# Kernel tuning notes

Hardware: AMD Instinct MI355X
Metric: run time of the kernel (lower is better)

Reference implementation:

```python
import jax, jax.numpy as jnp
import numpy as np

N_NODES = 100000
EPS = 1e-12  # F.normalize default eps


def _sage_conv(x, edge_index, Wl, bl, Wr):
    # PyG SAGEConv, aggr='mean', normalize=True.
    # edge_index[0] = source j, edge_index[1] = target i; messages flow j -> i.
    src, dst = edge_index[0], edge_index[1]
    msg_sum = jax.ops.segment_sum(x[src], dst, num_segments=N_NODES)  # [N, F]
    cnt = jax.ops.segment_sum(jnp.ones_like(src, dtype=x.dtype), dst,
                              num_segments=N_NODES)                  # [N]
    mean = msg_sum / jnp.maximum(cnt, 1.0)[:, None]  # empty neighborhoods -> 0
    out = mean @ Wl + bl + x @ Wr                    # lin_l(aggr) + lin_r(x)
    norm = jnp.sqrt(jnp.sum(out * out, axis=-1, keepdims=True))
    return out / jnp.maximum(norm, EPS)              # row-wise L2 normalize


def setup_inputs() -> dict:
    key = jax.random.key(0)
    ks = jax.random.split(key, 8)
    F_IN, F_HID, F_OUT = 64, 64, 32
    x = jax.random.normal(ks[0], (N_NODES, F_IN), dtype=jnp.float32)
    edge_index = jax.random.randint(ks[1], (2, 1000000), 0, N_NODES, dtype=jnp.int64)
    s1 = 1.0 / np.sqrt(F_IN)
    s2 = 1.0 / np.sqrt(F_HID)
    return {
        "x": x,
        "edge_index": edge_index,
        "W1l": jax.random.normal(ks[2], (F_IN, F_HID), dtype=jnp.float32) * s1,
        "b1": jnp.zeros((F_HID,), dtype=jnp.float32),
        "W1r": jax.random.normal(ks[3], (F_IN, F_HID), dtype=jnp.float32) * s1,
        "W2l": jax.random.normal(ks[4], (F_HID, F_OUT), dtype=jnp.float32) * s2,
        "b2": jnp.zeros((F_OUT,), dtype=jnp.float32),
        "W2r": jax.random.normal(ks[5], (F_HID, F_OUT), dtype=jnp.float32) * s2,
    }


def reference(x, edge_index, W1l, b1, W1r, W2l, b2, W2r):
    # eval mode: dropout(p=0.6) is identity
    h = jax.nn.relu(_sage_conv(x, edge_index, W1l, b1, W1r))
    out = _sage_conv(h, edge_index, W2l, b2, W2r)
    return out
```

## Files before the change

### kernel.cpp

```cpp
#include <hip/hip_runtime.h>

#define NN 100000
#define NE 1000000
#define NBK 391
#define CAP 3072
#define CH 8192
#define NCB ((NE + CH - 1) / CH)

typedef __attribute__((ext_vector_type(8))) short bf16x8;
typedef __attribute__((ext_vector_type(4))) float f32x4;

__device__ __forceinline__ ushort f2bf(float f) {
    uint u = __builtin_bit_cast(uint, f);
    u += 0x7FFFu + ((u >> 16) & 1u);
    return (ushort)(u >> 16);
}
__device__ __forceinline__ uint pack2(float a, float b) {
    uint ua = __builtin_bit_cast(uint, a), ub = __builtin_bit_cast(uint, b);
    ua += 0x7FFFu + ((ua >> 16) & 1u);
    ub += 0x7FFFu + ((ub >> 16) & 1u);
    return (ua >> 16) | (ub & 0xFFFF0000u);
}
__device__ __forceinline__ float blo(uint v) { return __builtin_bit_cast(float, v << 16); }
__device__ __forceinline__ float bhi(uint v) { return __builtin_bit_cast(float, v & 0xFFFF0000u); }

#define ACC8(u, v)                                                         \
    a0 += blo(u.x); a1 += bhi(u.x); a2 += blo(u.y); a3 += bhi(u.y);        \
    a4 += blo(u.z); a5 += bhi(u.z); a6 += blo(u.w); a7 += bhi(u.w);        \
    b0 += blo(v.x); b1 += bhi(v.x); b2 += blo(v.y); b3 += bhi(v.y);        \
    b4 += blo(v.z); b5 += bhi(v.z); b6 += blo(v.w); b7 += bhi(v.w);

__global__ void prep_all(const float* __restrict__ x, uint* __restrict__ xb2,
                         const float* __restrict__ W1l, const float* __restrict__ W1r,
                         const float* __restrict__ W2l, const float* __restrict__ W2r,
                         ushort* __restrict__ W1t, ushort* __restrict__ W2t,
                         int* __restrict__ gcur) {
    int t = blockIdx.x * blockDim.x + threadIdx.x;
    if (t < NN * 16) {
        float4 v = reinterpret_cast<const float4*>(x)[t];
        uint2 o;
        o.x = pack2(v.x, v.y);
        o.y = pack2(v.z, v.w);
        reinterpret_cast<uint2*>(xb2)[t] = o;
    } else {
        int u = t - NN * 16;
        if (u < 64 * 128) {
            int f = u >> 7, k = u & 127;
            float v = (k < 64) ? W1l[k * 64 + f] : W1r[(k - 64) * 64 + f];
            W1t[u] = f2bf(v);
        } else if (u < 64 * 128 + 32 * 128) {
            int p = u - 64 * 128;
            int f = p >> 7, k = p & 127;
            float v = (k < 64) ? W2l[k * 32 + f] : W2r[(k - 64) * 32 + f];
            W2t[p] = f2bf(v);
        } else if (u < 64 * 128 + 32 * 128 + NBK) {
            int b = u - 64 * 128 - 32 * 128;
            gcur[b] = b * CAP;
        }
    }
}

__global__ __launch_bounds__(512) void bin_edges(const int* __restrict__ src,
                                                 const int* __restrict__ dst,
                                                 int* __restrict__ gcur,
                                                 uint* __restrict__ binned) {
    __shared__ int lh[NBK + 1], lb[NBK + 1], lr[NBK + 1];
    int tid = threadIdx.x;
    for (int i = tid; i < NBK + 1; i += 512) { lh[i] = 0; lr[i] = 0; }
    __syncthreads();
    int base = blockIdx.x * CH;
#pragma unroll
    for (int k = 0; k < 16; ++k) {
        int e = base + tid + k * 512;
        if (e < NE) atomicAdd(&lh[dst[e] >> 8], 1);
    }
    __syncthreads();
    if (tid < NBK && lh[tid] > 0) lb[tid] = atomicAdd(&gcur[tid], lh[tid]);
    __syncthreads();
#pragma unroll
    for (int k = 0; k < 16; ++k) {
        int e = base + tid + k * 512;
        if (e < NE) {
            int d = dst[e];
            int bk = d >> 8;
            int r = atomicAdd(&lr[bk], 1);
            binned[lb[bk] + r] = (uint)src[e] | ((uint)(d & 255) << 24);
        }
    }
}

__global__ __launch_bounds__(256) void sort_bucket(const uint* __restrict__ binned,
                                                   const int* __restrict__ gcur,
                                                   uint* __restrict__ ssrc,
                                                   uint* __restrict__ offp) {
    __shared__ uint recs[CAP];
    __shared__ uint srt[CAP];
    __shared__ int cnt[256], sc[256], cur[256];
    int b = blockIdx.x, t = threadIdx.x;
    int s = b * CAP, n = gcur[b] - s;
    cnt[t] = 0;
    __syncthreads();
    for (int i = t; i < n; i += 256) {
        uint r = binned[s + i];
        recs[i] = r;
        atomicAdd(&cnt[r >> 24], 1);
    }
    __syncthreads();
    int c = cnt[t];
    sc[t] = c;
    for (int d = 1; d < 256; d <<= 1) {
        __syncthreads();
        int add = (t >= d) ? sc[t - d] : 0;
        __syncthreads();
        sc[t] += add;
    }
    __syncthreads();
    int ex = sc[t] - c;
    cur[t] = ex;
    int node = b * 256 + t;
    if (node < NN) offp[node] = (uint)(s + ex) | ((uint)c << 22);
    __syncthreads();
    for (int i = t; i < n; i += 256) {
        uint r = recs[i];
        int p = atomicAdd(&cur[r >> 24], 1);
        srt[p] = r & 0xFFFFFFu;
    }
    __syncthreads();
    for (int i = t; i < n; i += 256) ssrc[s + i] = srt[i];
}

__global__ __launch_bounds__(256) void layer1_fused(
    const uint4* __restrict__ xb4, const ushort* __restrict__ xb,
    const uint* __restrict__ offp, const uint* __restrict__ ssrc,
    const ushort* __restrict__ Wt, const float* __restrict__ bias,
    ushort* __restrict__ hb) {
    int w = threadIdx.x >> 6, l = threadIdx.x & 63;
    int r = l & 15, q = l >> 4;
    int node0 = blockIdx.x * 64 + w * 16;
    int node = node0 + r;
    int beg = 0, end = 0;
    if (node < NN) {
        uint p = offp[node];
        beg = (int)(p & 0x3FFFFFu);
        end = beg + (int)(p >> 22);
    }
    float a0=0.f,a1=0.f,a2=0.f,a3=0.f,a4=0.f,a5=0.f,a6=0.f,a7=0.f;
    float b0=0.f,b1=0.f,b2=0.f,b3=0.f,b4=0.f,b5=0.f,b6=0.f,b7=0.f;
    int i = beg;
    for (; i + 3 < end; i += 4) {
        uint j0 = ssrc[i], j1 = ssrc[i + 1], j2 = ssrc[i + 2], j3 = ssrc[i + 3];
        uint4 u0 = xb4[(size_t)j0 * 8 + q];
        uint4 v0 = xb4[(size_t)j0 * 8 + q + 4];
        uint4 u1 = xb4[(size_t)j1 * 8 + q];
        uint4 v1 = xb4[(size_t)j1 * 8 + q + 4];
        uint4 u2 = xb4[(size_t)j2 * 8 + q];
        uint4 v2 = xb4[(size_t)j2 * 8 + q + 4];
        uint4 u3 = xb4[(size_t)j3 * 8 + q];
        uint4 v3 = xb4[(size_t)j3 * 8 + q + 4];
        ACC8(u0, v0) ACC8(u1, v1) ACC8(u2, v2) ACC8(u3, v3)
    }
    for (; i < end; ++i) {
        uint j0 = ssrc[i];
        uint4 u0 = xb4[(size_t)j0 * 8 + q];
        uint4 v0 = xb4[(size_t)j0 * 8 + q + 4];
        ACC8(u0, v0)
    }
    float inv = 1.f / fmaxf((float)(end - beg), 1.f);
    uint4 mu, mv;
    mu.x = pack2(a0 * inv, a1 * inv); mu.y = pack2(a2 * inv, a3 * inv);
    mu.z = pack2(a4 * inv, a5 * inv); mu.w = pack2(a6 * inv, a7 * inv);
    mv.x = pack2(b0 * inv, b1 * inv); mv.y = pack2(b2 * inv, b3 * inv);
    mv.z = pack2(b4 * inv, b5 * inv); mv.w = pack2(b6 * inv, b7 * inv);
    bf16x8 afr0 = __builtin_bit_cast(bf16x8, mu);
    bf16x8 afr1 = __builtin_bit_cast(bf16x8, mv);
    int arow = (node < NN) ? node : NN - 1;
    const ushort* ax = xb + (size_t)arow * 64 + q * 8;
    bf16x8 afr2 = *reinterpret_cast<const bf16x8*>(ax);
    bf16x8 afr3 = *reinterpret_cast<const bf16x8*>(ax + 32);

    f32x4 c0 = {0.f, 0.f, 0.f, 0.f}, c1 = c0, c2 = c0, c3 = c0;
    const ushort* wp = Wt + (size_t)r * 128 + q * 8;
#pragma unroll
    for (int ks = 0; ks < 4; ++ks) {
        const ushort* wk = wp + ks * 32;
        bf16x8 w0 = *reinterpret_cast<const bf16x8*>(wk);
        bf16x8 w1 = *reinterpret_cast<const bf16x8*>(wk + 16 * 128);
        bf16x8 w2 = *reinterpret_cast<const bf16x8*>(wk + 32 * 128);
        bf16x8 w3 = *reinterpret_cast<const bf16x8*>(wk + 48 * 128);
        bf16x8 af = (ks == 0) ? afr0 : (ks == 1) ? afr1 : (ks == 2) ? afr2 : afr3;
        c0 = __builtin_amdgcn_mfma_f32_16x16x32_bf16(af, w0, c0, 0, 0, 0);
        c1 = __builtin_amdgcn_mfma_f32_16x16x32_bf16(af, w1, c1, 0, 0, 0);
        c2 = __builtin_amdgcn_mfma_f32_16x16x32_bf16(af, w2, c2, 0, 0, 0);
        c3 = __builtin_amdgcn_mfma_f32_16x16x32_bf16(af, w3, c3, 0, 0, 0);
    }
    float bb0 = bias[r], bb1 = bias[16 + r], bb2 = bias[32 + r], bb3 = bias[48 + r];
#pragma unroll
    for (int reg = 0; reg < 4; ++reg) {
        c0[reg] += bb0; c1[reg] += bb1; c2[reg] += bb2; c3[reg] += bb3;
    }
#pragma unroll
    for (int reg = 0; reg < 4; ++reg) {
        float s = c0[reg] * c0[reg] + c1[reg] * c1[reg] +
                  c2[reg] * c2[reg] + c3[reg] * c3[reg];
        s += __shfl_xor(s, 1, 64);
        s += __shfl_xor(s, 2, 64);
        s += __shfl_xor(s, 4, 64);
        s += __shfl_xor(s, 8, 64);
        float scl = 1.f / fmaxf(sqrtf(s), 1e-12f);
        int grow = node0 + q * 4 + reg;
        if (grow < NN) {
            ushort* hp = hb + (size_t)grow * 64 + r;
            hp[0]  = f2bf(fmaxf(c0[reg] * scl, 0.f));
            hp[16] = f2bf(fmaxf(c1[reg] * scl, 0.f));
            hp[32] = f2bf(fmaxf(c2[reg] * scl, 0.f));
            hp[48] = f2bf(fmaxf(c3[reg] * scl, 0.f));
        }
    }
}

__global__ __launch_bounds__(256) void layer2_fused(
    const uint4* __restrict__ hb4, const ushort* __restrict__ hbuf,
    const uint* __restrict__ offp, const uint* __restrict__ ssrc,
    const ushort* __restrict__ Wt, const float* __restrict__ bias,
    float* __restrict__ out) {
    int w = threadIdx.x >> 6, l = threadIdx.x & 63;
    int r = l & 15, q = l >> 4;
    int node0 = blockIdx.x * 64 + w * 16;
    int node = node0 + r;
    int beg = 0, end = 0;
    if (node < NN) {
        uint p = offp[node];
        beg = (int)(p & 0x3FFFFFu);
        end = beg + (int)(p >> 22);
    }
    float a0=0.f,a1=0.f,a2=0.f,a3=0.f,a4=0.f,a5=0.f,a6=0.f,a7=0.f;
    float b0=0.f,b1=0.f,b2=0.f,b3=0.f,b4=0.f,b5=0.f,b6=0.f,b7=0.f;
    int i = beg;
    for (; i + 3 < end; i += 4) {
        uint j0 = ssrc[i], j1 = ssrc[i + 1], j2 = ssrc[i + 2], j3 = ssrc[i + 3];
        uint4 u0 = hb4[(size_t)j0 * 8 + q];
        uint4 v0 = hb4[(size_t)j0 * 8 + q + 4];
        uint4 u1 = hb4[(size_t)j1 * 8 + q];
        uint4 v1 = hb4[(size_t)j1 * 8 + q + 4];
        uint4 u2 = hb4[(size_t)j2 * 8 + q];
        uint4 v2 = hb4[(size_t)j2 * 8 + q + 4];
        uint4 u3 = hb4[(size_t)j3 * 8 + q];
        uint4 v3 = hb4[(size_t)j3 * 8 + q + 4];
        ACC8(u0, v0) ACC8(u1, v1) ACC8(u2, v2) ACC8(u3, v3)
    }
    for (; i < end; ++i) {
        uint j0 = ssrc[i];
        uint4 u0 = hb4[(size_t)j0 * 8 + q];
        uint4 v0 = hb4[(size_t)j0 * 8 + q + 4];
        ACC8(u0, v0)
    }
    float inv = 1.f / fmaxf((float)(end - beg), 1.f);
    uint4 mu, mv;
    mu.x = pack2(a0 * inv, a1 * inv); mu.y = pack2(a2 * inv, a3 * inv);
    mu.z = pack2(a4 * inv, a5 * inv); mu.w = pack2(a6 * inv, a7 * inv);
    mv.x = pack2(b0 * inv, b1 * inv); mv.y = pack2(b2 * inv, b3 * inv);
    mv.z = pack2(b4 * inv, b5 * inv); mv.w = pack2(b6 * inv, b7 * inv);
    bf16x8 afr0 = __builtin_bit_cast(bf16x8, mu);
    bf16x8 afr1 = __builtin_bit_cast(bf16x8, mv);
    int arow = (node < NN) ? node : NN - 1;
    const ushort* ax = hbuf + (size_t)arow * 64 + q * 8;
    bf16x8 afr2 = *reinterpret_cast<const bf16x8*>(ax);
    bf16x8 afr3 = *reinterpret_cast<const bf16x8*>(ax + 32);

    f32x4 c0 = {0.f, 0.f, 0.f, 0.f}, c1 = c0;
    const ushort* wp = Wt + (size_t)r * 128 + q * 8;
#pragma unroll
    for (int ks = 0; ks < 4; ++ks) {
        const ushort* wk = wp + ks * 32;
        bf16x8 w0 = *reinterpret_cast<const bf16x8*>(wk);
        bf16x8 w1 = *reinterpret_cast<const bf16x8*>(wk + 16 * 128);
        bf16x8 af = (ks == 0) ? afr0 : (ks == 1) ? afr1 : (ks == 2) ? afr2 : afr3;
        c0 = __builtin_amdgcn_mfma_f32_16x16x32_bf16(af, w0, c0, 0, 0, 0);
        c1 = __builtin_amdgcn_mfma_f32_16x16x32_bf16(af, w1, c1, 0, 0, 0);
    }
    float bb0 = bias[r], bb1 = bias[16 + r];
#pragma unroll
    for (int reg = 0; reg < 4; ++reg) { c0[reg] += bb0; c1[reg] += bb1; }
#pragma unroll
    for (int reg = 0; reg < 4; ++reg) {
        float s = c0[reg] * c0[reg] + c1[reg] * c1[reg];
        s += __shfl_xor(s, 1, 64);
        s += __shfl_xor(s, 2, 64);
        s += __shfl_xor(s, 4, 64);
        s += __shfl_xor(s, 8, 64);
        float scl = 1.f / fmaxf(sqrtf(s), 1e-12f);
        int grow = node0 + q * 4 + reg;
        if (grow < NN) {
            float* op = out + (size_t)grow * 32 + r;
            op[0]  = c0[reg] * scl;
            op[16] = c1[reg] * scl;
        }
    }
}

extern "C" void kernel_launch(void* const* d_in, const int* in_sizes, int n_in,
                              void* d_out, int out_size, void* d_ws, size_t ws_size,
                              hipStream_t stream) {
    const float* x   = (const float*)d_in[0];
    const int*   ei  = (const int*)d_in[1];
    const int*   src = ei;
    const int*   dst = ei + NE;
    const float* W1l = (const float*)d_in[2];
    const float* b1  = (const float*)d_in[3];
    const float* W1r = (const float*)d_in[4];
    const float* W2l = (const float*)d_in[5];
    const float* b2  = (const float*)d_in[6];
    const float* W2r = (const float*)d_in[7];
    float* out = (float*)d_out;

    ushort* xb   = (ushort*)d_ws;
    ushort* hb   = xb + (size_t)NN * 64;
    ushort* W1t  = hb + (size_t)NN * 64;
    ushort* W2t  = W1t + 64 * 128;
    int*    gcur = (int*)(W2t + 32 * 128);
    uint*   offp = (uint*)(gcur + NBK + 1);
    uint*   binn = offp + NN;
    uint*   ssrc = binn + (size_t)NBK * CAP;

    prep_all    <<<(NN * 16 + 12288 + NBK + 255) / 256, 256, 0, stream>>>(
                    x, (uint*)xb, W1l, W1r, W2l, W2r, W1t, W2t, gcur);
    bin_edges   <<<NCB, 512, 0, stream>>>(src, dst, gcur, binn);
    sort_bucket <<<NBK, 256, 0, stream>>>(binn, gcur, ssrc, offp);

    layer1_fused<<<(NN + 63) / 64, 256, 0, stream>>>(
                    (const uint4*)xb, xb, offp, ssrc, W1t, b1, hb);
    layer2_fused<<<(NN + 63) / 64, 256, 0, stream>>>(
                    (const uint4*)hb, hb, offp, ssrc, W2t, b2, out);
}
```

Baseline: 114.2 us.

## Group nodes by in-degree within each bucket to balance per-wavefront gather loops

The sort kernel now builds a per-bucket permutation that orders the 256 nodes of each bucket by in-degree (capped at 63) using a counting sort in shared memory. Both layer kernels read node ids through this permutation, so the 16 nodes handled together in one wavefront have similar neighbor counts and loop trip counts. This is meant to cut lane idling from degree imbalance in the gather loops. The cost is an extra indirection load per node, scattered output row writes instead of contiguous ones, a little more work in the sort kernel, and 391 extra padding-node slots that are launched and then skipped.

```diff
diff --git a/kernel.cpp b/kernel.cpp
--- a/kernel.cpp
+++ b/kernel.cpp
@@ -3,6 +3,7 @@
 #define NN 100000
 #define NE 1000000
 #define NBK 391
+#define NPERM (NBK * 256)
 #define CAP 3072
 #define CH 8192
 #define NCB ((NE + CH - 1) / CH)
@@ -92,10 +93,12 @@
 __global__ __launch_bounds__(256) void sort_bucket(const uint* __restrict__ binned,
                                                    const int* __restrict__ gcur,
                                                    uint* __restrict__ ssrc,
-                                                   uint* __restrict__ offp) {
+                                                   uint* __restrict__ offp,
+                                                   int* __restrict__ perm) {
     __shared__ uint recs[CAP];
     __shared__ uint srt[CAP];
     __shared__ int cnt[256], sc[256], cur[256];
+    __shared__ int dcur[64];
     int b = blockIdx.x, t = threadIdx.x;
     int s = b * CAP, n = gcur[b] - s;
     cnt[t] = 0;
@@ -120,6 +123,24 @@
     int node = b * 256 + t;
     if (node < NN) offp[node] = (uint)(s + ex) | ((uint)c << 22);
     __syncthreads();
+    int dg = min(c, 63);
+    cnt[t] = 0;
+    __syncthreads();
+    atomicAdd(&cnt[dg], 1);
+    __syncthreads();
+    int dv = (t < 64) ? cnt[t] : 0;
+    sc[t] = dv;
+    for (int d = 1; d < 64; d <<= 1) {
+        __syncthreads();
+        int add = (t >= d && t < 64) ? sc[t - d] : 0;
+        __syncthreads();
+        if (t < 64) sc[t] += add;
+    }
+    __syncthreads();
+    if (t < 64) dcur[t] = sc[t] - dv;
+    __syncthreads();
+    int pos = atomicAdd(&dcur[dg], 1);
+    perm[b * 256 + pos] = node;
     for (int i = t; i < n; i += 256) {
         uint r = recs[i];
         int p = atomicAdd(&cur[r >> 24], 1);
@@ -132,12 +153,13 @@
 __global__ __launch_bounds__(256) void layer1_fused(
     const uint4* __restrict__ xb4, const ushort* __restrict__ xb,
     const uint* __restrict__ offp, const uint* __restrict__ ssrc,
+    const int* __restrict__ perm,
     const ushort* __restrict__ Wt, const float* __restrict__ bias,
     ushort* __restrict__ hb) {
     int w = threadIdx.x >> 6, l = threadIdx.x & 63;
     int r = l & 15, q = l >> 4;
     int node0 = blockIdx.x * 64 + w * 16;
-    int node = node0 + r;
+    int node = perm[node0 + r];
     int beg = 0, end = 0;
     if (node < NN) {
         uint p = offp[node];
@@ -173,7 +195,7 @@
     mv.z = pack2(b4 * inv, b5 * inv); mv.w = pack2(b6 * inv, b7 * inv);
     bf16x8 afr0 = __builtin_bit_cast(bf16x8, mu);
     bf16x8 afr1 = __builtin_bit_cast(bf16x8, mv);
-    int arow = (node < NN) ? node : NN - 1;
+    int arow = (node < NN) ? node : 0;
     const ushort* ax = xb + (size_t)arow * 64 + q * 8;
     bf16x8 afr2 = *reinterpret_cast<const bf16x8*>(ax);
     bf16x8 afr3 = *reinterpret_cast<const bf16x8*>(ax + 32);
@@ -207,9 +229,9 @@
         s += __shfl_xor(s, 4, 64);
         s += __shfl_xor(s, 8, 64);
         float scl = 1.f / fmaxf(sqrtf(s), 1e-12f);
-        int grow = node0 + q * 4 + reg;
-        if (grow < NN) {
-            ushort* hp = hb + (size_t)grow * 64 + r;
+        int prow = __shfl(node, q * 4 + reg, 16);
+        if (prow < NN) {
+            ushort* hp = hb + (size_t)prow * 64 + r;
             hp[0]  = f2bf(fmaxf(c0[reg] * scl, 0.f));
             hp[16] = f2bf(fmaxf(c1[reg] * scl, 0.f));
             hp[32] = f2bf(fmaxf(c2[reg] * scl, 0.f));
@@ -221,12 +243,13 @@
 __global__ __launch_bounds__(256) void layer2_fused(
     const uint4* __restrict__ hb4, const ushort* __restrict__ hbuf,
     const uint* __restrict__ offp, const uint* __restrict__ ssrc,
+    const int* __restrict__ perm,
     const ushort* __restrict__ Wt, const float* __restrict__ bias,
     float* __restrict__ out) {
     int w = threadIdx.x >> 6, l = threadIdx.x & 63;
     int r = l & 15, q = l >> 4;
     int node0 = blockIdx.x * 64 + w * 16;
-    int node = node0 + r;
+    int node = perm[node0 + r];
     int beg = 0, end = 0;
     if (node < NN) {
         uint p = offp[node];
@@ -262,7 +285,7 @@
     mv.z = pack2(b4 * inv, b5 * inv); mv.w = pack2(b6 * inv, b7 * inv);
     bf16x8 afr0 = __builtin_bit_cast(bf16x8, mu);
     bf16x8 afr1 = __builtin_bit_cast(bf16x8, mv);
-    int arow = (node < NN) ? node : NN - 1;
+    int arow = (node < NN) ? node : 0;
     const ushort* ax = hbuf + (size_t)arow * 64 + q * 8;
     bf16x8 afr2 = *reinterpret_cast<const bf16x8*>(ax);
     bf16x8 afr3 = *reinterpret_cast<const bf16x8*>(ax + 32);
@@ -289,9 +312,9 @@
         s += __shfl_xor(s, 4, 64);
         s += __shfl_xor(s, 8, 64);
         float scl = 1.f / fmaxf(sqrtf(s), 1e-12f);
-        int grow = node0 + q * 4 + reg;
-        if (grow < NN) {
-            float* op = out + (size_t)grow * 32 + r;
+        int prow = __shfl(node, q * 4 + reg, 16);
+        if (prow < NN) {
+            float* op = out + (size_t)prow * 32 + r;
             op[0]  = c0[reg] * scl;
             op[16] = c1[reg] * scl;
         }
@@ -319,16 +342,17 @@
     ushort* W2t  = W1t + 64 * 128;
     int*    gcur = (int*)(W2t + 32 * 128);
     uint*   offp = (uint*)(gcur + NBK + 1);
-    uint*   binn = offp + NN;
+    int*    perm = (int*)(offp + NN);
+    uint*   binn = (uint*)(perm + NPERM);
     uint*   ssrc = binn + (size_t)NBK * CAP;
 
     prep_all    <<<(NN * 16 + 12288 + NBK + 255) / 256, 256, 0, stream>>>(
                     x, (uint*)xb, W1l, W1r, W2l, W2r, W1t, W2t, gcur);
     bin_edges   <<<NCB, 512, 0, stream>>>(src, dst, gcur, binn);
-    sort_bucket <<<NBK, 256, 0, stream>>>(binn, gcur, ssrc, offp);
-
-    layer1_fused<<<(NN + 63) / 64, 256, 0, stream>>>(
-                    (const uint4*)xb, xb, offp, ssrc, W1t, b1, hb);
-    layer2_fused<<<(NN + 63) / 64, 256, 0, stream>>>(
-                    (const uint4*)hb, hb, offp, ssrc, W2t, b2, out);
-}
+    sort_bucket <<<NBK, 256, 0, stream>>>(binn, gcur, ssrc, offp, perm);
+
+    layer1_fused<<<NPERM / 64, 256, 0, stream>>>(
+                    (const uint4*)xb, xb, offp, ssrc, perm, W1t, b1, hb);
+    layer2_fused<<<NPERM / 64, 256, 0, stream>>>(
+                    (const uint4*)hb, hb, offp, ssrc, perm, W2t, b2, out);
+}
```

After: 123.0 us. 1.08x slower.

## Fuse prep and edge binning, pad neighbor lists to multiples of four

Applied to the files above, without the earlier changes.

Merges the feature/weight conversion kernel and the edge binning kernel into one launch, replacing the in-kernel gcur init with a memset and making bucket offsets relative. Sort_bucket pads each node's neighbor list to a multiple of four with a dummy zero row (index NN), writes directly to global without the shared staging buffer, and the layer kernels drop the scalar tail loop and software-prefetch the next index group. The added zero rows in xb/hb and a larger bucket capacity support the padding, at the cost of extra gathers of the dummy row and uncoalesced scatter writes to ssrc.

```diff
diff --git a/kernel.cpp b/kernel.cpp
--- a/kernel.cpp
+++ b/kernel.cpp
@@ -3,9 +3,11 @@
 #define NN 100000
 #define NE 1000000
 #define NBK 391
-#define CAP 3072
+#define CAP 3328
 #define CH 8192
 #define NCB ((NE + CH - 1) / CH)
+#define PREP_ITEMS (NN * 16 + 32 + 64 * 128 + 32 * 128)
+#define NPREPB ((PREP_ITEMS + 511) / 512)
 
 typedef __attribute__((ext_vector_type(8))) short bf16x8;
 typedef __attribute__((ext_vector_type(4))) float f32x4;
@@ -30,12 +32,42 @@
     b0 += blo(v.x); b1 += bhi(v.x); b2 += blo(v.y); b3 += bhi(v.y);        \
     b4 += blo(v.z); b5 += bhi(v.z); b6 += blo(v.w); b7 += bhi(v.w);
 
-__global__ void prep_all(const float* __restrict__ x, uint* __restrict__ xb2,
-                         const float* __restrict__ W1l, const float* __restrict__ W1r,
-                         const float* __restrict__ W2l, const float* __restrict__ W2r,
-                         ushort* __restrict__ W1t, ushort* __restrict__ W2t,
-                         int* __restrict__ gcur) {
-    int t = blockIdx.x * blockDim.x + threadIdx.x;
+__global__ __launch_bounds__(512) void prep_bin(
+    const float* __restrict__ x, uint* __restrict__ xb2,
+    const float* __restrict__ W1l, const float* __restrict__ W1r,
+    const float* __restrict__ W2l, const float* __restrict__ W2r,
+    ushort* __restrict__ W1t, ushort* __restrict__ W2t,
+    uint* __restrict__ hb2,
+    const int* __restrict__ src, const int* __restrict__ dst,
+    int* __restrict__ gcur, uint* __restrict__ binned) {
+    int tid = threadIdx.x;
+    if (blockIdx.x < NCB) {
+        __shared__ int lh[NBK + 1], lb[NBK + 1], lr[NBK + 1];
+        for (int i = tid; i < NBK + 1; i += 512) { lh[i] = 0; lr[i] = 0; }
+        __syncthreads();
+        int base = blockIdx.x * CH;
+#pragma unroll
+        for (int k = 0; k < 16; ++k) {
+            int e = base + tid + k * 512;
+            if (e < NE) atomicAdd(&lh[dst[e] >> 8], 1);
+        }
+        __syncthreads();
+        if (tid < NBK && lh[tid] > 0)
+            lb[tid] = tid * CAP + atomicAdd(&gcur[tid], lh[tid]);
+        __syncthreads();
+#pragma unroll
+        for (int k = 0; k < 16; ++k) {
+            int e = base + tid + k * 512;
+            if (e < NE) {
+                int d = dst[e];
+                int bk = d >> 8;
+                int r = atomicAdd(&lr[bk], 1);
+                binned[lb[bk] + r] = (uint)src[e] | ((uint)(d & 255) << 24);
+            }
+        }
+        return;
+    }
+    int t = (blockIdx.x - NCB) * 512 + tid;
     if (t < NN * 16) {
         float4 v = reinterpret_cast<const float4*>(x)[t];
         uint2 o;
@@ -43,48 +75,25 @@
         o.y = pack2(v.z, v.w);
         reinterpret_cast<uint2*>(xb2)[t] = o;
     } else {
-        int u = t - NN * 16;
-        if (u < 64 * 128) {
-            int f = u >> 7, k = u & 127;
-            float v = (k < 64) ? W1l[k * 64 + f] : W1r[(k - 64) * 64 + f];
-            W1t[u] = f2bf(v);
-        } else if (u < 64 * 128 + 32 * 128) {
-            int p = u - 64 * 128;
-            int f = p >> 7, k = p & 127;
-            float v = (k < 64) ? W2l[k * 32 + f] : W2r[(k - 64) * 32 + f];
-            W2t[p] = f2bf(v);
-        } else if (u < 64 * 128 + 32 * 128 + NBK) {
-            int b = u - 64 * 128 - 32 * 128;
-            gcur[b] = b * CAP;
-        }
-    }
-}
-
-__global__ __launch_bounds__(512) void bin_edges(const int* __restrict__ src,
-                                                 const int* __restrict__ dst,
-                                                 int* __restrict__ gcur,
-                                                 uint* __restrict__ binned) {
-    __shared__ int lh[NBK + 1], lb[NBK + 1], lr[NBK + 1];
-    int tid = threadIdx.x;
-    for (int i = tid; i < NBK + 1; i += 512) { lh[i] = 0; lr[i] = 0; }
-    __syncthreads();
-    int base = blockIdx.x * CH;
-#pragma unroll
-    for (int k = 0; k < 16; ++k) {
-        int e = base + tid + k * 512;
-        if (e < NE) atomicAdd(&lh[dst[e] >> 8], 1);
-    }
-    __syncthreads();
-    if (tid < NBK && lh[tid] > 0) lb[tid] = atomicAdd(&gcur[tid], lh[tid]);
-    __syncthreads();
-#pragma unroll
-    for (int k = 0; k < 16; ++k) {
-        int e = base + tid + k * 512;
-        if (e < NE) {
-            int d = dst[e];
-            int bk = d >> 8;
-            int r = atomicAdd(&lr[bk], 1);
-            binned[lb[bk] + r] = (uint)src[e] | ((uint)(d & 255) << 24);
+        int z = t - NN * 16;
+        if (z < 16) {
+            uint2 o; o.x = 0u; o.y = 0u;
+            reinterpret_cast<uint2*>(xb2)[NN * 16 + z] = o;
+        } else if (z < 32) {
+            uint2 o; o.x = 0u; o.y = 0u;
+            reinterpret_cast<uint2*>(hb2)[NN * 16 + (z - 16)] = o;
+        } else {
+            int u = z - 32;
+            if (u < 64 * 128) {
+                int f = u >> 7, k = u & 127;
+                float v = (k < 64) ? W1l[k * 64 + f] : W1r[(k - 64) * 64 + f];
+                W1t[u] = f2bf(v);
+            } else if (u < 64 * 128 + 32 * 128) {
+                int p = u - 64 * 128;
+                int f = p >> 7, k = p & 127;
+                float v = (k < 64) ? W2l[k * 32 + f] : W2r[(k - 64) * 32 + f];
+                W2t[p] = f2bf(v);
+            }
         }
     }
 }
@@ -94,10 +103,9 @@
                                                    uint* __restrict__ ssrc,
                                                    uint* __restrict__ offp) {
     __shared__ uint recs[CAP];
-    __shared__ uint srt[CAP];
     __shared__ int cnt[256], sc[256], cur[256];
     int b = blockIdx.x, t = threadIdx.x;
-    int s = b * CAP, n = gcur[b] - s;
+    int s = b * CAP, n = gcur[b];
     cnt[t] = 0;
     __syncthreads();
     for (int i = t; i < n; i += 256) {
@@ -107,7 +115,8 @@
     }
     __syncthreads();
     int c = cnt[t];
-    sc[t] = c;
+    int pc = (c + 3) & ~3;
+    sc[t] = pc;
     for (int d = 1; d < 256; d <<= 1) {
         __syncthreads();
         int add = (t >= d) ? sc[t - d] : 0;
@@ -115,7 +124,7 @@
         sc[t] += add;
     }
     __syncthreads();
-    int ex = sc[t] - c;
+    int ex = sc[t] - pc;
     cur[t] = ex;
     int node = b * 256 + t;
     if (node < NN) offp[node] = (uint)(s + ex) | ((uint)c << 22);
@@ -123,10 +132,9 @@
     for (int i = t; i < n; i += 256) {
         uint r = recs[i];
         int p = atomicAdd(&cur[r >> 24], 1);
-        srt[p] = r & 0xFFFFFFu;
-    }
-    __syncthreads();
-    for (int i = t; i < n; i += 256) ssrc[s + i] = srt[i];
+        ssrc[s + p] = r & 0xFFFFFFu;
+    }
+    for (int z = ex + c; z < ex + pc; ++z) ssrc[s + z] = NN;
 }
 
 __global__ __launch_bounds__(256) void layer1_fused(
@@ -138,17 +146,19 @@
     int r = l & 15, q = l >> 4;
     int node0 = blockIdx.x * 64 + w * 16;
     int node = node0 + r;
-    int beg = 0, end = 0;
+    int beg = 0, c = 0;
     if (node < NN) {
         uint p = offp[node];
         beg = (int)(p & 0x3FFFFFu);
-        end = beg + (int)(p >> 22);
-    }
+        c = (int)(p >> 22);
+    }
+    int rem = (c + 3) & ~3;
     float a0=0.f,a1=0.f,a2=0.f,a3=0.f,a4=0.f,a5=0.f,a6=0.f,a7=0.f;
     float b0=0.f,b1=0.f,b2=0.f,b3=0.f,b4=0.f,b5=0.f,b6=0.f,b7=0.f;
     int i = beg;
-    for (; i + 3 < end; i += 4) {
-        uint j0 = ssrc[i], j1 = ssrc[i + 1], j2 = ssrc[i + 2], j3 = ssrc[i + 3];
+    uint j0 = 0, j1 = 0, j2 = 0, j3 = 0;
+    if (rem > 0) { j0 = ssrc[i]; j1 = ssrc[i+1]; j2 = ssrc[i+2]; j3 = ssrc[i+3]; }
+    while (rem > 0) {
         uint4 u0 = xb4[(size_t)j0 * 8 + q];
         uint4 v0 = xb4[(size_t)j0 * 8 + q + 4];
         uint4 u1 = xb4[(size_t)j1 * 8 + q];
@@ -157,15 +167,11 @@
         uint4 v2 = xb4[(size_t)j2 * 8 + q + 4];
         uint4 u3 = xb4[(size_t)j3 * 8 + q];
         uint4 v3 = xb4[(size_t)j3 * 8 + q + 4];
+        i += 4; rem -= 4;
+        if (rem > 0) { j0 = ssrc[i]; j1 = ssrc[i+1]; j2 = ssrc[i+2]; j3 = ssrc[i+3]; }
         ACC8(u0, v0) ACC8(u1, v1) ACC8(u2, v2) ACC8(u3, v3)
     }
-    for (; i < end; ++i) {
-        uint j0 = ssrc[i];
-        uint4 u0 = xb4[(size_t)j0 * 8 + q];
-        uint4 v0 = xb4[(size_t)j0 * 8 + q + 4];
-        ACC8(u0, v0)
-    }
-    float inv = 1.f / fmaxf((float)(end - beg), 1.f);
+    float inv = 1.f / fmaxf((float)c, 1.f);
     uint4 mu, mv;
     mu.x = pack2(a0 * inv, a1 * inv); mu.y = pack2(a2 * inv, a3 * inv);
     mu.z = pack2(a4 * inv, a5 * inv); mu.w = pack2(a6 * inv, a7 * inv);
@@ -173,7 +179,7 @@
     mv.z = pack2(b4 * inv, b5 * inv); mv.w = pack2(b6 * inv, b7 * inv);
     bf16x8 afr0 = __builtin_bit_cast(bf16x8, mu);
     bf16x8 afr1 = __builtin_bit_cast(bf16x8, mv);
-    int arow = (node < NN) ? node : NN - 1;
+    int arow = (node < NN) ? node : 0;
     const ushort* ax = xb + (size_t)arow * 64 + q * 8;
     bf16x8 afr2 = *reinterpret_cast<const bf16x8*>(ax);
     bf16x8 afr3 = *reinterpret_cast<const bf16x8*>(ax + 32);
@@ -227,17 +233,19 @@
     int r = l & 15, q = l >> 4;
     int node0 = blockIdx.x * 64 + w * 16;
     int node = node0 + r;
-    int beg = 0, end = 0;
+    int beg = 0, c = 0;
     if (node < NN) {
         uint p = offp[node];
         beg = (int)(p & 0x3FFFFFu);
-        end = beg + (int)(p >> 22);
-    }
+        c = (int)(p >> 22);
+    }
+    int rem = (c + 3) & ~3;
     float a0=0.f,a1=0.f,a2=0.f,a3=0.f,a4=0.f,a5=0.f,a6=0.f,a7=0.f;
     float b0=0.f,b1=0.f,b2=0.f,b3=0.f,b4=0.f,b5=0.f,b6=0.f,b7=0.f;
     int i = beg;
-    for (; i + 3 < end; i += 4) {
-        uint j0 = ssrc[i], j1 = ssrc[i + 1], j2 = ssrc[i + 2], j3 = ssrc[i + 3];
+    uint j0 = 0, j1 = 0, j2 = 0, j3 = 0;
+    if (rem > 0) { j0 = ssrc[i]; j1 = ssrc[i+1]; j2 = ssrc[i+2]; j3 = ssrc[i+3]; }
+    while (rem > 0) {
         uint4 u0 = hb4[(size_t)j0 * 8 + q];
         uint4 v0 = hb4[(size_t)j0 * 8 + q + 4];
         uint4 u1 = hb4[(size_t)j1 * 8 + q];
@@ -246,15 +254,11 @@
         uint4 v2 = hb4[(size_t)j2 * 8 + q + 4];
         uint4 u3 = hb4[(size_t)j3 * 8 + q];
         uint4 v3 = hb4[(size_t)j3 * 8 + q + 4];
+        i += 4; rem -= 4;
+        if (rem > 0) { j0 = ssrc[i]; j1 = ssrc[i+1]; j2 = ssrc[i+2]; j3 = ssrc[i+3]; }
         ACC8(u0, v0) ACC8(u1, v1) ACC8(u2, v2) ACC8(u3, v3)
     }
-    for (; i < end; ++i) {
-        uint j0 = ssrc[i];
-        uint4 u0 = hb4[(size_t)j0 * 8 + q];
-        uint4 v0 = hb4[(size_t)j0 * 8 + q + 4];
-        ACC8(u0, v0)
-    }
-    float inv = 1.f / fmaxf((float)(end - beg), 1.f);
+    float inv = 1.f / fmaxf((float)c, 1.f);
     uint4 mu, mv;
     mu.x = pack2(a0 * inv, a1 * inv); mu.y = pack2(a2 * inv, a3 * inv);
     mu.z = pack2(a4 * inv, a5 * inv); mu.w = pack2(a6 * inv, a7 * inv);
@@ -262,7 +266,7 @@
     mv.z = pack2(b4 * inv, b5 * inv); mv.w = pack2(b6 * inv, b7 * inv);
     bf16x8 afr0 = __builtin_bit_cast(bf16x8, mu);
     bf16x8 afr1 = __builtin_bit_cast(bf16x8, mv);
-    int arow = (node < NN) ? node : NN - 1;
+    int arow = (node < NN) ? node : 0;
     const ushort* ax = hbuf + (size_t)arow * 64 + q * 8;
     bf16x8 afr2 = *reinterpret_cast<const bf16x8*>(ax);
     bf16x8 afr3 = *reinterpret_cast<const bf16x8*>(ax + 32);
@@ -314,18 +318,20 @@
     float* out = (float*)d_out;
 
     ushort* xb   = (ushort*)d_ws;
-    ushort* hb   = xb + (size_t)NN * 64;
-    ushort* W1t  = hb + (size_t)NN * 64;
+    ushort* hb   = xb + (size_t)(NN + 1) * 64;
+    ushort* W1t  = hb + (size_t)(NN + 1) * 64;
     ushort* W2t  = W1t + 64 * 128;
     int*    gcur = (int*)(W2t + 32 * 128);
     uint*   offp = (uint*)(gcur + NBK + 1);
-    uint*   binn = offp + NN;
+    uint*   binn = (uint*)(offp + NN);
     uint*   ssrc = binn + (size_t)NBK * CAP;
 
-    prep_all    <<<(NN * 16 + 12288 + NBK + 255) / 256, 256, 0, stream>>>(
-                    x, (uint*)xb, W1l, W1r, W2l, W2r, W1t, W2t, gcur);
-    bin_edges   <<<NCB, 512, 0, stream>>>(src, dst, gcur, binn);
-    sort_bucket <<<NBK, 256, 0, stream>>>(binn, gcur, ssrc, offp);
+    hipMemsetAsync(gcur, 0, (NBK + 1) * sizeof(int), stream);
+
+    prep_bin   <<<NCB + NPREPB, 512, 0, stream>>>(
+                   x, (uint*)xb, W1l, W1r, W2l, W2r, W1t, W2t, (uint*)hb,
+                   src, dst, gcur, binn);
+    sort_bucket<<<NBK, 256, 0, stream>>>(binn, gcur, ssrc, offp);
 
     layer1_fused<<<(NN + 63) / 64, 256, 0, stream>>>(
                     (const uint4*)xb, xb, offp, ssrc, W1t, b1, hb);
```

After: 112.0 us. Within noise of the previous version (-1.9%).
